# Kernel optimization log

Hardware: AMD Instinct MI355X
Metric: run time of the kernel (lower is better)

## Reference

```python
import jax, jax.numpy as jnp
import numpy as np

N, T, V, F, K, FO = 8, 64, 200, 64, 3, 64


def setup_inputs() -> dict:
    key = jax.random.key(0)
    k1, k2, k3, k4 = jax.random.split(key, 4)
    x = jax.random.normal(k1, (N, T, V, F), dtype=jnp.float32)
    Att = jax.random.uniform(k2, (N, V, V), dtype=jnp.float32)
    S = jax.random.uniform(k3, (N, T, V, V), dtype=jnp.float32)
    Theta = jax.random.normal(k4, (K, F, FO), dtype=jnp.float32) * 0.1
    return {"x": x, "Att": Att, "S": S, "Theta": Theta}


def reference(x, Att, S, Theta):
    # x: (N,T,V,F); Att: (N,V,V); S: (N,T,V,V); Theta: (K,F,FO)
    n, t, v, f = x.shape
    k_order = Theta.shape[0]
    # symmetrize S by elementwise min with its transpose (last two dims)
    S = jnp.minimum(S, jnp.swapaxes(S, -1, -2))
    eye = jnp.eye(v, dtype=x.dtype)
    # D = diag_embed(sum(A, dim=1)) per timestep -> column sums over axis 2
    d = jnp.sum(S, axis=2)                      # (N,T,V)
    L = d[..., :, None] * eye - S               # (N,T,V,V), D - A
    L_t = L - eye                               # tilde-L
    # Chebyshev recursion (elementwise, matching original code exactly)
    polys = [jnp.broadcast_to(eye, (1, 1, v, v)), L_t][:k_order]
    for _ in range(2, k_order):
        polys.append(2.0 * L_t * polys[-1] - polys[-2])
    Att_b = Att[:, None]                        # (N,1,V,V), broadcast over T
    out = jnp.zeros((n, t, v, Theta.shape[-1]), dtype=x.dtype)
    for kk in range(k_order):
        T_k_att = polys[kk] * Att_b             # (N,T,V,V) (broadcast for k=0)
        # rhs = T_k_att^T @ x : sum over vertex u
        rhs = jnp.einsum('...uv,...uf->...vf', T_k_att, x)  # (N,T,V,F)
        out = out + rhs @ Theta[kk]             # (N,T,V,FO)
    return jax.nn.relu(out)
```

## Files before the change

kernel.cpp:

```cpp
#include <hip/hip_runtime.h>

namespace {

typedef __attribute__((ext_vector_type(8)))  short          short8;
typedef __attribute__((ext_vector_type(8)))  unsigned short u16x8;
typedef __attribute__((ext_vector_type(4)))  unsigned short u16x4;
typedef __attribute__((ext_vector_type(4)))  float          f32x4;

constexpr int V   = 200;
constexpr int VP  = 208;
constexpr int UP  = 224;
constexpr int F   = 64;
constexpr int FO  = 64;
constexpr int NT  = 512;

constexpr size_t WS_SMIN  = 0;
constexpr size_t WS_D     = 47710208;
constexpr size_t WS_SDIAG = 48136192;
constexpr size_t WS_ATTT  = 48562176;
constexpr size_t WS_ADIAG = 50167808;
constexpr size_t WS_THT   = 50174976;

__device__ __forceinline__ unsigned short f2bf(float x) {
    union { float f; unsigned u; } c; c.f = x;
    unsigned r = c.u + 0x7FFF + ((c.u >> 16) & 1);
    return (unsigned short)(r >> 16);
}
__device__ __forceinline__ float bf2f(unsigned short h) {
    union { unsigned u; float f; } c; c.u = ((unsigned)h) << 16;
    return c.f;
}

__global__ __launch_bounds__(256)
void prep_smin(const float* __restrict__ S,
               unsigned short* __restrict__ smin,
               float* __restrict__ d_ws,
               float* __restrict__ sdiag)
{
    __shared__ float As[32][33];
    __shared__ float Bs[32][33];
    __shared__ float Ms[32][33];

    const int b   = blockIdx.x;
    const int tid = threadIdx.x;
    int rem = blockIdx.y, ti = 0;
    while (rem >= 7 - ti) { rem -= 7 - ti; ++ti; }
    const int tj = ti + rem;
    const bool diag = (ti == tj);

    const float* __restrict__ Sp = S + (size_t)b * (V * V);
    unsigned short* __restrict__ smp = smin + (size_t)b * (VP * UP);

    const int r  = tid >> 3;
    const int cg = tid & 7;
    const int c0 = 4 * cg;

    {
        const int gr = 32 * ti + r, gc = 32 * tj + c0;
        float4 a = make_float4(0.f, 0.f, 0.f, 0.f);
        if (gr < V && gc < V) a = *(const float4*)&Sp[gr * V + gc];
        As[r][c0 + 0] = a.x; As[r][c0 + 1] = a.y; As[r][c0 + 2] = a.z; As[r][c0 + 3] = a.w;
        if (!diag) {
            const int hr = 32 * tj + r, hc = 32 * ti + c0;
            float4 bb = make_float4(0.f, 0.f, 0.f, 0.f);
            if (hr < V && hc < V) bb = *(const float4*)&Sp[hr * V + hc];
            Bs[r][c0 + 0] = bb.x; Bs[r][c0 + 1] = bb.y; Bs[r][c0 + 2] = bb.z; Bs[r][c0 + 3] = bb.w;
        }
    }
    __syncthreads();

    float m[4], rs = 0.f;
    #pragma unroll
    for (int e = 0; e < 4; ++e) {
        const int c = c0 + e;
        const float tw = diag ? As[c][r] : Bs[c][r];
        m[e] = fminf(As[r][c], tw);
        Ms[r][c] = m[e];
        rs += m[e];
    }
    rs += __shfl_xor(rs, 1); rs += __shfl_xor(rs, 2); rs += __shfl_xor(rs, 4);
    if (cg == 0 && 32 * ti + r < V)
        atomicAdd(&d_ws[b * VP + 32 * ti + r], rs);
    if (diag && cg == 0 && 32 * ti + r < V)
        sdiag[b * VP + 32 * ti + r] = As[r][r];
    __syncthreads();

    if (!diag) {
        float ts = 0.f;
        #pragma unroll
        for (int e = 0; e < 4; ++e) ts += Ms[c0 + e][r];
        ts += __shfl_xor(ts, 1); ts += __shfl_xor(ts, 2); ts += __shfl_xor(ts, 4);
        if (cg == 0 && 32 * tj + r < V)
            atomicAdd(&d_ws[b * VP + 32 * tj + r], ts);
    }

    {
        const int vr = 32 * ti + r;
        if (vr < VP) {
            u16x4 w;
            #pragma unroll
            for (int e = 0; e < 4; ++e) w[e] = f2bf(m[e]);
            *(u16x4*)&smp[vr * UP + 32 * tj + c0] = w;
        }
        if (!diag) {
            const int vr2 = 32 * tj + r;
            if (vr2 < VP) {
                u16x4 w2;
                #pragma unroll
                for (int e = 0; e < 4; ++e) w2[e] = f2bf(Ms[c0 + e][r]);
                *(u16x4*)&smp[vr2 * UP + 32 * ti + c0] = w2;
            }
        }
    }
}

__global__ __launch_bounds__(256)
void prep_att(const float* __restrict__ Att,
              float* __restrict__ attT,
              float* __restrict__ adiag)
{
    __shared__ float T[32][33];
    const int n  = blockIdx.x;
    const int ut = blockIdx.y / 7, vt = blockIdx.y % 7;
    const int tid = threadIdx.x;

    for (int idx = tid; idx < 1024; idx += 256) {
        const int rr = idx >> 5, cc = idx & 31;
        const int u = 32 * ut + rr, v = 32 * vt + cc;
        T[rr][cc] = (u < V && v < V) ? Att[(size_t)n * (V * V) + u * V + v] : 0.f;
    }
    __syncthreads();
    for (int idx = tid; idx < 1024; idx += 256) {
        const int r2 = idx >> 5, c2 = idx & 31;
        attT[(size_t)n * (UP * UP) + (32 * vt + r2) * UP + 32 * ut + c2] = T[c2][r2];
    }
    if (ut == vt && tid < 32)
        adiag[n * UP + 32 * vt + tid] = T[tid][tid];
}

__global__ __launch_bounds__(256)
void prep_theta(const float* __restrict__ Theta,
                unsigned short* __restrict__ thT)
{
    __shared__ float T[64][65];
    const int k = blockIdx.x, tid = threadIdx.x;
    for (int idx = tid; idx < 4096; idx += 256)
        T[idx >> 6][idx & 63] = Theta[k * 4096 + idx];
    __syncthreads();
    for (int idx = tid; idx < 4096; idx += 256) {
        const int fo = idx >> 6, f = idx & 63;
        thT[k * 4096 + fo * 64 + f] = f2bf(T[f][fo]);
    }
}

constexpr int XS_S = 68;
constexpr int A_S  = 40;
constexpr int YS_S = 72;

__global__ __launch_bounds__(256, 2)
void cheb_main(const float* __restrict__ x,
               const unsigned short* __restrict__ thT,
               const unsigned short* __restrict__ smin,
               const float* __restrict__ d_ws,
               const float* __restrict__ sdiag,
               const float* __restrict__ attT,
               const float* __restrict__ adiag,
               float* __restrict__ out)
{
    __shared__ __align__(16) char smem[65408];
    unsigned short* xs  = (unsigned short*)smem;
    unsigned short* A1  = (unsigned short*)(smem + 30464);
    unsigned short* A2  = (unsigned short*)(smem + 47104);
    unsigned short* ys  = (unsigned short*)smem;
    unsigned short* ThS = (unsigned short*)(smem + 30464);
    float*        cbuf  = (float*)(smem + 63744);
    float*       adbuf  = (float*)(smem + 64576);

    const int tid = threadIdx.x;
    const int b   = blockIdx.x;
    const int n   = b >> 6;
    const float* __restrict__ xp = x + (size_t)b * (V * F);
    const unsigned short* __restrict__ sm = smin + (size_t)b * (VP * UP);
    const float* __restrict__ atp = attT + (size_t)n * (UP * UP);
    float* __restrict__ op = out + (size_t)b * (V * FO);

    for (int idx = tid; idx < UP * 16; idx += 256) {
        const int u = idx >> 4, fg = idx & 15;
        u16x4 w; w[0] = 0; w[1] = 0; w[2] = 0; w[3] = 0;
        if (u < V) {
            const float4 v = *(const float4*)&xp[u * F + 4 * fg];
            w[0] = f2bf(v.x); w[1] = f2bf(v.y); w[2] = f2bf(v.z); w[3] = f2bf(v.w);
        }
        *(u16x4*)&xs[u * XS_S + 4 * fg] = w;
    }
    if (tid < VP) {
        cbuf[tid]  = d_ws[b * VP + tid] - 1.0f - sdiag[b * VP + tid];
        adbuf[tid] = adiag[n * UP + tid];
    }

    const int wave = tid >> 6, lane = tid & 63;
    const int q = lane >> 4, ln = lane & 15;
    const int myBase = (wave == 0) ? 0 : (4 + 3 * (wave - 1));
    const int myCnt  = (wave == 0) ? 4 : 3;

    f32x4 acc1[4][4], acc2[4][4];
    #pragma unroll
    for (int i = 0; i < 4; ++i)
        #pragma unroll
        for (int j = 0; j < 4; ++j) {
            acc1[i][j] = (f32x4)0.f; acc2[i][j] = (f32x4)0.f;
        }

    u16x8 pf_s[4]; float4 pf_a0[4], pf_a1[4];
    auto load_chunks = [&](int kt) {
        const int u0 = 32 * kt;
        #pragma unroll
        for (int c = 0; c < 4; ++c) {
            const int idx = tid + 256 * c;
            if (idx < VP * 4) {
                const int v = idx >> 2, ch = idx & 3;
                const int u8 = u0 + 8 * ch;
                pf_s[c]  = *(const u16x8*)&sm[v * UP + u8];
                pf_a0[c] = *(const float4*)&atp[v * UP + u8];
                pf_a1[c] = *(const float4*)&atp[v * UP + u8 + 4];
            }
        }
    };
    load_chunks(0);

    for (int kt = 0; kt < 7; ++kt) {
        const int u0 = 32 * kt;
        __syncthreads();
        #pragma unroll
        for (int c = 0; c < 4; ++c) {
            const int idx = tid + 256 * c;
            if (idx < VP * 4) {
                const int v = idx >> 2, ch = idx & 3;
                const int u8 = u0 + 8 * ch;
                const u16x8 s8 = pf_s[c];
                const float att[8] = {pf_a0[c].x, pf_a0[c].y, pf_a0[c].z, pf_a0[c].w,
                                      pf_a1[c].x, pf_a1[c].y, pf_a1[c].z, pf_a1[c].w};
                u16x8 w1, w2;
                #pragma unroll
                for (int jj = 0; jj < 8; ++jj) {
                    const float m = bf2f(s8[jj]);
                    if (u8 + jj == v) { w1[jj] = 0; w2[jj] = 0; }
                    else {
                        w1[jj] = f2bf(-m * att[jj]);
                        w2[jj] = f2bf(2.0f * m * m * att[jj]);
                    }
                }
                *(u16x8*)&A1[v * A_S + 8 * ch] = w1;
                *(u16x8*)&A2[v * A_S + 8 * ch] = w2;
            }
        }
        if (kt < 6) load_chunks(kt + 1);
        __syncthreads();
        short8 bfr[4];
        #pragma unroll
        for (int ft = 0; ft < 4; ++ft)
            #pragma unroll
            for (int j = 0; j < 8; ++j)
                bfr[ft][j] = (short)xs[(u0 + 8 * q + j) * XS_S + 16 * ft + ln];
        #pragma unroll
        for (int vi = 0; vi < 4; ++vi) {
            if (vi < myCnt) {
                const int row = (myBase + vi) * 16 + ln;
                const short8 af1 = *(const short8*)&A1[row * A_S + 8 * q];
                const short8 af2 = *(const short8*)&A2[row * A_S + 8 * q];
                #pragma unroll
                for (int ft = 0; ft < 4; ++ft) {
                    acc1[vi][ft] = __builtin_amdgcn_mfma_f32_16x16x32_bf16(af1, bfr[ft], acc1[vi][ft], 0, 0, 0);
                    acc2[vi][ft] = __builtin_amdgcn_mfma_f32_16x16x32_bf16(af2, bfr[ft], acc2[vi][ft], 0, 0, 0);
                }
            }
        }
    }

    f32x4 ot[4][4];
    #pragma unroll
    for (int i = 0; i < 4; ++i)
        #pragma unroll
        for (int j = 0; j < 4; ++j) ot[i][j] = (f32x4)0.f;

    #pragma unroll
    for (int pass = 0; pass < 3; ++pass) {
        const int k = (pass == 0) ? 1 : (pass == 1) ? 2 : 0;
        __syncthreads();

        if (k == 0) {
            for (int idx = tid; idx < VP * 16; idx += 256) {
                const int v = idx >> 4, fg = idx & 15;
                u16x4 w; w[0] = 0; w[1] = 0; w[2] = 0; w[3] = 0;
                if (v < V) {
                    const float av = adbuf[v];
                    const float4 xv = *(const float4*)&xp[v * F + 4 * fg];
                    w[0] = f2bf(av * xv.x); w[1] = f2bf(av * xv.y);
                    w[2] = f2bf(av * xv.z); w[3] = f2bf(av * xv.w);
                }
                *(u16x4*)&ys[v * YS_S + 4 * fg] = w;
            }
        } else {
            #pragma unroll
            for (int vi = 0; vi < 4; ++vi) {
                if (vi < myCnt) {
                    const int vt = myBase + vi;
                    #pragma unroll
                    for (int ft = 0; ft < 4; ++ft) {
                        const f32x4 a = (k == 1) ? acc1[vi][ft] : acc2[vi][ft];
                        #pragma unroll
                        for (int reg = 0; reg < 4; ++reg) {
                            const int v = vt * 16 + 4 * q + reg;
                            float val = 0.f;
                            if (v < V) {
                                const float cc = cbuf[v];
                                const float dc = ((k == 1) ? cc : (2.0f * cc * cc - 1.0f)) * adbuf[v];
                                val = a[reg] + dc * xp[v * F + 16 * ft + ln];
                            }
                            ys[v * YS_S + 16 * ft + ln] = f2bf(val);
                        }
                    }
                }
            }
        }
        for (int idx = tid; idx < 64 * 8; idx += 256) {
            const int fo = idx >> 3, ch = idx & 7;
            *(u16x8*)&ThS[fo * YS_S + 8 * ch] =
                *(const u16x8*)&thT[k * 4096 + fo * 64 + 8 * ch];
        }
        __syncthreads();
        #pragma unroll
        for (int vi = 0; vi < 4; ++vi) {
            if (vi < myCnt) {
                const int vrow = (myBase + vi) * 16 + ln;
                #pragma unroll
                for (int ks = 0; ks < 2; ++ks) {
                    const short8 af = *(const short8*)&ys[vrow * YS_S + 32 * ks + 8 * q];
                    #pragma unroll
                    for (int fot = 0; fot < 4; ++fot) {
                        const short8 bf = *(const short8*)&ThS[(16 * fot + ln) * YS_S + 32 * ks + 8 * q];
                        ot[vi][fot] = __builtin_amdgcn_mfma_f32_16x16x32_bf16(af, bf, ot[vi][fot], 0, 0, 0);
                    }
                }
            }
        }
    }

    #pragma unroll
    for (int vi = 0; vi < 4; ++vi) {
        if (vi < myCnt) {
            const int vt = myBase + vi;
            #pragma unroll
            for (int fot = 0; fot < 4; ++fot) {
                #pragma unroll
                for (int reg = 0; reg < 4; ++reg) {
                    const int v = vt * 16 + 4 * q + reg;
                    if (v < V)
                        op[v * FO + 16 * fot + ln] = fmaxf(ot[vi][fot][reg], 0.f);
                }
            }
        }
    }
}

}

extern "C" void kernel_launch(void* const* d_in, const int* in_sizes, int n_in,
                              void* d_out, int out_size, void* d_ws, size_t ws_size,
                              hipStream_t stream) {
    const float* x     = (const float*)d_in[0];
    const float* Att   = (const float*)d_in[1];
    const float* S     = (const float*)d_in[2];
    const float* Theta = (const float*)d_in[3];
    float* out         = (float*)d_out;

    char* ws = (char*)d_ws;
    unsigned short* smin = (unsigned short*)(ws + WS_SMIN);
    float* d_sum = (float*)(ws + WS_D);
    float* sdiag = (float*)(ws + WS_SDIAG);
    float* attT  = (float*)(ws + WS_ATTT);
    float* adiag = (float*)(ws + WS_ADIAG);
    unsigned short* thT = (unsigned short*)(ws + WS_THT);

    hipMemsetAsync(d_sum, 0, (size_t)NT * VP * sizeof(float), stream);

    hipLaunchKernelGGL(prep_smin,  dim3(NT, 28), dim3(256), 0, stream, S, smin, d_sum, sdiag);
    hipLaunchKernelGGL(prep_att,   dim3(8, 49),  dim3(256), 0, stream, Att, attT, adiag);
    hipLaunchKernelGGL(prep_theta, dim3(3),      dim3(256), 0, stream, Theta, thT);
    hipLaunchKernelGGL(cheb_main,  dim3(NT),     dim3(256), 0, stream,
                       x, thT, smin, d_sum, sdiag, attT, adiag, out);
}
```

Measured before the change: 237.1 us.

## Precompute bf16 A1/A2 operands in prep kernel, stream MFMA fragments directly

The elementwise products of S_min with Att (the L_t*Att and 2*L_t^2*Att off-diagonal terms) now happen in the S-symmetrizing prep kernel. That kernel writes bf16 A1/A2 in a chunked per-row layout that the main kernel loads straight into MFMA A-fragments from global memory, double-buffered in registers. This removes the per-tile LDS staging, the conversion work and two barriers per k-tile in cheb_main. x is also transposed once in LDS so B fragments become vector loads. In exchange, the workspace traffic for the A operands doubles (two bf16 matrices instead of one bf16 plus a shared fp32 Att), and Att is re-read for every timestep in prep.

```diff
diff --git a/kernel.cpp b/kernel.cpp
--- a/kernel.cpp
+++ b/kernel.cpp
@@ -14,12 +14,13 @@
 constexpr int FO  = 64;
 constexpr int NT  = 512;
 
-constexpr size_t WS_SMIN  = 0;
-constexpr size_t WS_D     = 47710208;
-constexpr size_t WS_SDIAG = 48136192;
-constexpr size_t WS_ATTT  = 48562176;
-constexpr size_t WS_ADIAG = 50167808;
-constexpr size_t WS_THT   = 50174976;
+constexpr int A_ROW = 448;
+
+constexpr size_t WS_AC  = 0;
+constexpr size_t WS_D   = 95420416;
+constexpr size_t WS_SD  = 95846400;
+constexpr size_t WS_AD  = 96272384;
+constexpr size_t WS_THT = 96279552;
 
 __device__ __forceinline__ unsigned short f2bf(float x) {
     union { float f; unsigned u; } c; c.f = x;
@@ -32,24 +33,27 @@
 }
 
 __global__ __launch_bounds__(256)
-void prep_smin(const float* __restrict__ S,
-               unsigned short* __restrict__ smin,
-               float* __restrict__ d_ws,
-               float* __restrict__ sdiag)
+void prep_A(const float* __restrict__ S,
+            const float* __restrict__ Att,
+            unsigned short* __restrict__ Ac,
+            float* __restrict__ d_ws,
+            float* __restrict__ sdiag)
 {
     __shared__ float As[32][33];
     __shared__ float Bs[32][33];
-    __shared__ float Ms[32][33];
+    __shared__ float Ts[32][33];
+    __shared__ float Us[32][33];
 
     const int b   = blockIdx.x;
+    const int n   = b >> 6;
     const int tid = threadIdx.x;
     int rem = blockIdx.y, ti = 0;
     while (rem >= 7 - ti) { rem -= 7 - ti; ++ti; }
     const int tj = ti + rem;
     const bool diag = (ti == tj);
 
-    const float* __restrict__ Sp = S + (size_t)b * (V * V);
-    unsigned short* __restrict__ smp = smin + (size_t)b * (VP * UP);
+    const float* __restrict__ Sp = S   + (size_t)b * (V * V);
+    const float* __restrict__ Ap = Att + (size_t)n * (V * V);
 
     const int r  = tid >> 3;
     const int cg = tid & 7;
@@ -58,84 +62,87 @@
     {
         const int gr = 32 * ti + r, gc = 32 * tj + c0;
         float4 a = make_float4(0.f, 0.f, 0.f, 0.f);
-        if (gr < V && gc < V) a = *(const float4*)&Sp[gr * V + gc];
+        float4 t = make_float4(0.f, 0.f, 0.f, 0.f);
+        if (gr < V && gc < V) {
+            a = *(const float4*)&Sp[gr * V + gc];
+            t = *(const float4*)&Ap[gr * V + gc];
+        }
         As[r][c0 + 0] = a.x; As[r][c0 + 1] = a.y; As[r][c0 + 2] = a.z; As[r][c0 + 3] = a.w;
+        Ts[r][c0 + 0] = t.x; Ts[r][c0 + 1] = t.y; Ts[r][c0 + 2] = t.z; Ts[r][c0 + 3] = t.w;
         if (!diag) {
             const int hr = 32 * tj + r, hc = 32 * ti + c0;
             float4 bb = make_float4(0.f, 0.f, 0.f, 0.f);
-            if (hr < V && hc < V) bb = *(const float4*)&Sp[hr * V + hc];
+            float4 uu = make_float4(0.f, 0.f, 0.f, 0.f);
+            if (hr < V && hc < V) {
+                bb = *(const float4*)&Sp[hr * V + hc];
+                uu = *(const float4*)&Ap[hr * V + hc];
+            }
             Bs[r][c0 + 0] = bb.x; Bs[r][c0 + 1] = bb.y; Bs[r][c0 + 2] = bb.z; Bs[r][c0 + 3] = bb.w;
+            Us[r][c0 + 0] = uu.x; Us[r][c0 + 1] = uu.y; Us[r][c0 + 2] = uu.z; Us[r][c0 + 3] = uu.w;
         }
     }
     __syncthreads();
-
-    float m[4], rs = 0.f;
-    #pragma unroll
-    for (int e = 0; e < 4; ++e) {
-        const int c = c0 + e;
-        const float tw = diag ? As[c][r] : Bs[c][r];
-        m[e] = fminf(As[r][c], tw);
-        Ms[r][c] = m[e];
-        rs += m[e];
-    }
-    rs += __shfl_xor(rs, 1); rs += __shfl_xor(rs, 2); rs += __shfl_xor(rs, 4);
-    if (cg == 0 && 32 * ti + r < V)
-        atomicAdd(&d_ws[b * VP + 32 * ti + r], rs);
-    if (diag && cg == 0 && 32 * ti + r < V)
-        sdiag[b * VP + 32 * ti + r] = As[r][r];
-    __syncthreads();
-
-    if (!diag) {
-        float ts = 0.f;
-        #pragma unroll
-        for (int e = 0; e < 4; ++e) ts += Ms[c0 + e][r];
-        ts += __shfl_xor(ts, 1); ts += __shfl_xor(ts, 2); ts += __shfl_xor(ts, 4);
-        if (cg == 0 && 32 * tj + r < V)
-            atomicAdd(&d_ws[b * VP + 32 * tj + r], ts);
-    }
 
     {
         const int vr = 32 * ti + r;
+        float rs = 0.f;
+        u16x4 w1, w2;
+        #pragma unroll
+        for (int e = 0; e < 4; ++e) {
+            const int c = c0 + e;
+            const float tw = diag ? As[c][r] : Bs[c][r];
+            const float m  = fminf(As[r][c], tw);
+            rs += m;
+            const float att = diag ? Ts[c][r] : Us[c][r];
+            float a1 = -m * att;
+            float a2 = 2.0f * m * m * att;
+            if (diag && r == c) { a1 = 0.f; a2 = 0.f; }
+            w1[e] = f2bf(a1); w2[e] = f2bf(a2);
+        }
+        float s = rs;
+        s += __shfl_xor(s, 1); s += __shfl_xor(s, 2); s += __shfl_xor(s, 4);
+        if (cg == 0 && vr < V)
+            atomicAdd(&d_ws[b * VP + vr], s);
+        if (diag && cg == 0 && vr < V)
+            sdiag[b * VP + vr] = As[r][r];
         if (vr < VP) {
-            u16x4 w;
-            #pragma unroll
-            for (int e = 0; e < 4; ++e) w[e] = f2bf(m[e]);
-            *(u16x4*)&smp[vr * UP + 32 * tj + c0] = w;
-        }
-        if (!diag) {
-            const int vr2 = 32 * tj + r;
-            if (vr2 < VP) {
-                u16x4 w2;
-                #pragma unroll
-                for (int e = 0; e < 4; ++e) w2[e] = f2bf(Ms[c0 + e][r]);
-                *(u16x4*)&smp[vr2 * UP + 32 * ti + c0] = w2;
-            }
+            const size_t base = ((size_t)(b * VP + vr) * 7 + tj) * 64;
+            *(u16x4*)&Ac[base + c0]      = w1;
+            *(u16x4*)&Ac[base + 32 + c0] = w2;
+        }
+    }
+
+    if (!diag) {
+        const int vr2 = 32 * tj + r;
+        float ts = 0.f;
+        u16x4 w1, w2;
+        #pragma unroll
+        for (int e = 0; e < 4; ++e) {
+            const int c = c0 + e;
+            const float m = fminf(Bs[r][c], As[c][r]);
+            ts += m;
+            const float att = Ts[c][r];
+            w1[e] = f2bf(-m * att);
+            w2[e] = f2bf(2.0f * m * m * att);
+        }
+        float s = ts;
+        s += __shfl_xor(s, 1); s += __shfl_xor(s, 2); s += __shfl_xor(s, 4);
+        if (cg == 0 && vr2 < V)
+            atomicAdd(&d_ws[b * VP + vr2], s);
+        if (vr2 < VP) {
+            const size_t base = ((size_t)(b * VP + vr2) * 7 + ti) * 64;
+            *(u16x4*)&Ac[base + c0]      = w1;
+            *(u16x4*)&Ac[base + 32 + c0] = w2;
         }
     }
 }
 
 __global__ __launch_bounds__(256)
-void prep_att(const float* __restrict__ Att,
-              float* __restrict__ attT,
-              float* __restrict__ adiag)
+void prep_adiag(const float* __restrict__ Att, float* __restrict__ adiag)
 {
-    __shared__ float T[32][33];
-    const int n  = blockIdx.x;
-    const int ut = blockIdx.y / 7, vt = blockIdx.y % 7;
-    const int tid = threadIdx.x;
-
-    for (int idx = tid; idx < 1024; idx += 256) {
-        const int rr = idx >> 5, cc = idx & 31;
-        const int u = 32 * ut + rr, v = 32 * vt + cc;
-        T[rr][cc] = (u < V && v < V) ? Att[(size_t)n * (V * V) + u * V + v] : 0.f;
-    }
-    __syncthreads();
-    for (int idx = tid; idx < 1024; idx += 256) {
-        const int r2 = idx >> 5, c2 = idx & 31;
-        attT[(size_t)n * (UP * UP) + (32 * vt + r2) * UP + 32 * ut + c2] = T[c2][r2];
-    }
-    if (ut == vt && tid < 32)
-        adiag[n * UP + 32 * vt + tid] = T[tid][tid];
+    const int n = blockIdx.x, tid = threadIdx.x;
+    if (tid < UP)
+        adiag[n * UP + tid] = (tid < V) ? Att[(size_t)n * (V * V) + tid * V + tid] : 0.f;
 }
 
 __global__ __launch_bounds__(256)
@@ -154,34 +161,31 @@
 }
 
 constexpr int XS_S = 68;
-constexpr int A_S  = 40;
+constexpr int XT_S = 232;
 constexpr int YS_S = 72;
 
 __global__ __launch_bounds__(256, 2)
 void cheb_main(const float* __restrict__ x,
                const unsigned short* __restrict__ thT,
-               const unsigned short* __restrict__ smin,
+               const unsigned short* __restrict__ Ac,
                const float* __restrict__ d_ws,
                const float* __restrict__ sdiag,
-               const float* __restrict__ attT,
                const float* __restrict__ adiag,
                float* __restrict__ out)
 {
-    __shared__ __align__(16) char smem[65408];
-    unsigned short* xs  = (unsigned short*)smem;
-    unsigned short* A1  = (unsigned short*)(smem + 30464);
-    unsigned short* A2  = (unsigned short*)(smem + 47104);
-    unsigned short* ys  = (unsigned short*)smem;
-    unsigned short* ThS = (unsigned short*)(smem + 30464);
-    float*        cbuf  = (float*)(smem + 63744);
-    float*       adbuf  = (float*)(smem + 64576);
+    __shared__ __align__(16) char smem[61824];
+    unsigned short* xsT = (unsigned short*)smem;
+    unsigned short* xs  = (unsigned short*)(smem + 29696);
+    unsigned short* ThS = (unsigned short*)smem;
+    unsigned short* ys  = (unsigned short*)(smem + 29696);
+    float*        cbuf  = (float*)(smem + 60160);
+    float*       adbuf  = (float*)(smem + 60992);
 
     const int tid = threadIdx.x;
     const int b   = blockIdx.x;
     const int n   = b >> 6;
     const float* __restrict__ xp = x + (size_t)b * (V * F);
-    const unsigned short* __restrict__ sm = smin + (size_t)b * (VP * UP);
-    const float* __restrict__ atp = attT + (size_t)n * (UP * UP);
+    const unsigned short* __restrict__ ap = Ac + (size_t)b * (VP * A_ROW);
     float* __restrict__ op = out + (size_t)b * (V * FO);
 
     for (int idx = tid; idx < UP * 16; idx += 256) {
@@ -197,6 +201,17 @@
         cbuf[tid]  = d_ws[b * VP + tid] - 1.0f - sdiag[b * VP + tid];
         adbuf[tid] = adiag[n * UP + tid];
     }
+    __syncthreads();
+
+    for (int it = 0; it < 7; ++it) {
+        const int wid = tid + 256 * it;
+        const int f = wid & 63, uc = wid >> 6;
+        u16x8 w;
+        #pragma unroll
+        for (int j = 0; j < 8; ++j) w[j] = xs[(8 * uc + j) * XS_S + f];
+        *(u16x8*)&xsT[f * XT_S + 8 * uc] = w;
+    }
+    __syncthreads();
 
     const int wave = tid >> 6, lane = tid & 63;
     const int q = lane >> 4, ln = lane & 15;
@@ -211,70 +226,40 @@
             acc1[i][j] = (f32x4)0.f; acc2[i][j] = (f32x4)0.f;
         }
 
-    u16x8 pf_s[4]; float4 pf_a0[4], pf_a1[4];
-    auto load_chunks = [&](int kt) {
-        const int u0 = 32 * kt;
-        #pragma unroll
-        for (int c = 0; c < 4; ++c) {
-            const int idx = tid + 256 * c;
-            if (idx < VP * 4) {
-                const int v = idx >> 2, ch = idx & 3;
-                const int u8 = u0 + 8 * ch;
-                pf_s[c]  = *(const u16x8*)&sm[v * UP + u8];
-                pf_a0[c] = *(const float4*)&atp[v * UP + u8];
-                pf_a1[c] = *(const float4*)&atp[v * UP + u8 + 4];
-            }
-        }
-    };
-    load_chunks(0);
-
+    size_t rbase[4];
+    #pragma unroll
+    for (int vi = 0; vi < 4; ++vi)
+        rbase[vi] = (size_t)((myBase + vi) * 16 + ln) * A_ROW;
+
+    short8 a1c[4] = {}, a2c[4] = {}, a1n[4] = {}, a2n[4] = {};
+    #pragma unroll
+    for (int vi = 0; vi < 4; ++vi) if (vi < myCnt) {
+        a1c[vi] = *(const short8*)&ap[rbase[vi] + 8 * q];
+        a2c[vi] = *(const short8*)&ap[rbase[vi] + 32 + 8 * q];
+    }
+    #pragma unroll 1
     for (int kt = 0; kt < 7; ++kt) {
-        const int u0 = 32 * kt;
-        __syncthreads();
-        #pragma unroll
-        for (int c = 0; c < 4; ++c) {
-            const int idx = tid + 256 * c;
-            if (idx < VP * 4) {
-                const int v = idx >> 2, ch = idx & 3;
-                const int u8 = u0 + 8 * ch;
-                const u16x8 s8 = pf_s[c];
-                const float att[8] = {pf_a0[c].x, pf_a0[c].y, pf_a0[c].z, pf_a0[c].w,
-                                      pf_a1[c].x, pf_a1[c].y, pf_a1[c].z, pf_a1[c].w};
-                u16x8 w1, w2;
-                #pragma unroll
-                for (int jj = 0; jj < 8; ++jj) {
-                    const float m = bf2f(s8[jj]);
-                    if (u8 + jj == v) { w1[jj] = 0; w2[jj] = 0; }
-                    else {
-                        w1[jj] = f2bf(-m * att[jj]);
-                        w2[jj] = f2bf(2.0f * m * m * att[jj]);
-                    }
-                }
-                *(u16x8*)&A1[v * A_S + 8 * ch] = w1;
-                *(u16x8*)&A2[v * A_S + 8 * ch] = w2;
-            }
-        }
-        if (kt < 6) load_chunks(kt + 1);
-        __syncthreads();
+        if (kt < 6) {
+            #pragma unroll
+            for (int vi = 0; vi < 4; ++vi) if (vi < myCnt) {
+                a1n[vi] = *(const short8*)&ap[rbase[vi] + (kt + 1) * 64 + 8 * q];
+                a2n[vi] = *(const short8*)&ap[rbase[vi] + (kt + 1) * 64 + 32 + 8 * q];
+            }
+        }
         short8 bfr[4];
         #pragma unroll
         for (int ft = 0; ft < 4; ++ft)
+            bfr[ft] = *(const short8*)&xsT[(16 * ft + ln) * XT_S + 32 * kt + 8 * q];
+        #pragma unroll
+        for (int vi = 0; vi < 4; ++vi) if (vi < myCnt) {
             #pragma unroll
-            for (int j = 0; j < 8; ++j)
-                bfr[ft][j] = (short)xs[(u0 + 8 * q + j) * XS_S + 16 * ft + ln];
-        #pragma unroll
-        for (int vi = 0; vi < 4; ++vi) {
-            if (vi < myCnt) {
-                const int row = (myBase + vi) * 16 + ln;
-                const short8 af1 = *(const short8*)&A1[row * A_S + 8 * q];
-                const short8 af2 = *(const short8*)&A2[row * A_S + 8 * q];
-                #pragma unroll
-                for (int ft = 0; ft < 4; ++ft) {
-                    acc1[vi][ft] = __builtin_amdgcn_mfma_f32_16x16x32_bf16(af1, bfr[ft], acc1[vi][ft], 0, 0, 0);
-                    acc2[vi][ft] = __builtin_amdgcn_mfma_f32_16x16x32_bf16(af2, bfr[ft], acc2[vi][ft], 0, 0, 0);
-                }
-            }
-        }
+            for (int ft = 0; ft < 4; ++ft) {
+                acc1[vi][ft] = __builtin_amdgcn_mfma_f32_16x16x32_bf16(a1c[vi], bfr[ft], acc1[vi][ft], 0, 0, 0);
+                acc2[vi][ft] = __builtin_amdgcn_mfma_f32_16x16x32_bf16(a2c[vi], bfr[ft], acc2[vi][ft], 0, 0, 0);
+            }
+        }
+        #pragma unroll
+        for (int vi = 0; vi < 4; ++vi) { a1c[vi] = a1n[vi]; a2c[vi] = a2n[vi]; }
     }
 
     f32x4 ot[4][4];
@@ -375,18 +360,17 @@
     float* out         = (float*)d_out;
 
     char* ws = (char*)d_ws;
-    unsigned short* smin = (unsigned short*)(ws + WS_SMIN);
-    float* d_sum = (float*)(ws + WS_D);
-    float* sdiag = (float*)(ws + WS_SDIAG);
-    float* attT  = (float*)(ws + WS_ATTT);
-    float* adiag = (float*)(ws + WS_ADIAG);
+    unsigned short* Ac  = (unsigned short*)(ws + WS_AC);
+    float* d_sum        = (float*)(ws + WS_D);
+    float* sdiag        = (float*)(ws + WS_SD);
+    float* adiag        = (float*)(ws + WS_AD);
     unsigned short* thT = (unsigned short*)(ws + WS_THT);
 
     hipMemsetAsync(d_sum, 0, (size_t)NT * VP * sizeof(float), stream);
 
-    hipLaunchKernelGGL(prep_smin,  dim3(NT, 28), dim3(256), 0, stream, S, smin, d_sum, sdiag);
-    hipLaunchKernelGGL(prep_att,   dim3(8, 49),  dim3(256), 0, stream, Att, attT, adiag);
+    hipLaunchKernelGGL(prep_A,     dim3(NT, 28), dim3(256), 0, stream, S, Att, Ac, d_sum, sdiag);
+    hipLaunchKernelGGL(prep_adiag, dim3(8),      dim3(256), 0, stream, Att, adiag);
     hipLaunchKernelGGL(prep_theta, dim3(3),      dim3(256), 0, stream, Theta, thT);
     hipLaunchKernelGGL(cheb_main,  dim3(NT),     dim3(256), 0, stream,
-                       x, thT, smin, d_sum, sdiag, attT, adiag, out);
-}
+                       x, thT, Ac, d_sum, sdiag, adiag, out);
+}
```

Result: slower. 247.5 us (+4.4%).
